# Kernel tuning notes

Measured on AMD Instinct MI355X. Metric: run time of the kernel, lower is better.

The kernel has to match this reference:

```python
import jax, jax.numpy as jnp
import numpy as np

N = 20000        # number of nodes
E_RAND = 140000  # random edges; self-loops appended to match original (neighbors.extend([curr_node]))
D_IN = 512
D_OUT = 512
SLOPE = 0.2


def setup_inputs() -> dict:
    key = jax.random.key(0)
    k1, k2, k3, k4 = jax.random.split(key, 4)
    nodes = jax.random.normal(k1, (N, D_IN), dtype=jnp.float32)
    ei = jax.random.randint(k2, (2, E_RAND), 0, N, dtype=jnp.int64)
    loops = jnp.arange(N, dtype=jnp.int64)
    edge_index = jnp.concatenate([ei, jnp.stack([loops, loops])], axis=1)  # [2, E_RAND+N]
    # learned params: nn.Linear(input_dim, output_dim) and nn.Linear(2*output_dim, 1)
    W = jax.random.normal(k3, (D_IN, D_OUT), dtype=jnp.float32) * (1.0 / np.sqrt(D_IN))
    b_w = jnp.zeros((D_OUT,), dtype=jnp.float32)
    a = jax.random.normal(k4, (2 * D_OUT,), dtype=jnp.float32) * (1.0 / np.sqrt(2 * D_OUT))
    b_a = jnp.zeros((), dtype=jnp.float32)
    return {"nodes": nodes, "edge_index": edge_index, "W": W, "b_w": b_w, "a": a, "b_a": b_a}


def reference(nodes, edge_index, W, b_w, a, b_a):
    # h = W x  (nn.Linear)
    h = nodes @ W + b_w                       # [N, D_OUT]
    src = edge_index[0]                       # neighbor j
    dst = edge_index[1]                       # center   i
    # a([h_i || h_j]) split into per-node partial scores (avoids materializing concat)
    s_dst = h @ a[:D_OUT]                     # [N]
    s_src = h @ a[D_OUT:]                     # [N]
    e = jax.nn.leaky_relu(s_dst[dst] + s_src[src] + b_a, negative_slope=SLOPE)  # [E]
    w = jnp.exp(e)                            # original uses exp without max-shift
    denom = jax.ops.segment_sum(w, dst, num_segments=N)       # [N]
    alpha = w / denom[dst]                    # per-edge softmax weight
    out = jax.ops.segment_sum(alpha[:, None] * h[src], dst, num_segments=N)  # [N, D_OUT]
    return out
```

## Files before the change

### kernel.cpp

```cpp
#include <hip/hip_runtime.h>
#include <stdint.h>

#define D 512
#define SLOPE 0.2f
#define ELLW 64

typedef unsigned short u16;
typedef u16 u16x8 __attribute__((ext_vector_type(8)));
typedef __bf16 bf16x8 __attribute__((ext_vector_type(8)));
typedef float f32x4 __attribute__((ext_vector_type(4)));

__device__ inline float bf2f(u16 b) {
    union { uint32_t u; float f; } v; v.u = ((uint32_t)b) << 16; return v.f;
}
__device__ inline u16 f2bf(float f) {
    union { uint32_t u; float f; } v; v.f = f;
    uint32_t u = v.u;
    if ((u & 0x7F800000u) == 0x7F800000u) return (u16)(u >> 16);
    uint32_t r = u + 0x7FFFu + ((u >> 16) & 1u);
    return (u16)(r >> 16);
}
__device__ inline void load8(const void* X, int isf32, size_t base, float* o) {
    if (isf32) {
        const float4* p = (const float4*)((const float*)X + base);
        float4 a = p[0], b = p[1];
        o[0] = a.x; o[1] = a.y; o[2] = a.z; o[3] = a.w;
        o[4] = b.x; o[5] = b.y; o[6] = b.z; o[7] = b.w;
    } else {
        u16x8 v = *(const u16x8*)((const u16*)X + base);
#pragma unroll
        for (int j = 0; j < 8; j++) o[j] = bf2f(v[j]);
    }
}
__device__ inline float load1(const void* X, int isf32, size_t idx) {
    return isf32 ? ((const float*)X)[idx] : bf2f(((const u16*)X)[idx]);
}
__device__ inline int eload(const void* ei, int is64, size_t idx) {
    return is64 ? (int)((const long long*)ei)[idx] : ((const int*)ei)[idx];
}

__global__ void fill_constf(float* __restrict__ out, float val, int n) {
    int i = blockIdx.x * 256 + threadIdx.x;
    if (i < n) out[i] = val;
}

__global__ void detect2_kernel(const u16* __restrict__ xr, const uint32_t* __restrict__ er,
                               const void* __restrict__ ei, int* __restrict__ flags,
                               int nx, int newords, int E, int Nn) {
    __shared__ int cnt_band, cnt_zero, bad;
    int t = threadIdx.x;
    if (t == 0) { cnt_band = 0; cnt_zero = 0; bad = 0; }
    __syncthreads();
    {
        size_t stride = (size_t)nx / 256;
        size_t idx = ((size_t)t * stride) & ~(size_t)1;
        u16 v = xr[idx];
        int e = (v >> 7) & 0xFF;
        if (e >= 100 && e <= 140) atomicAdd(&cnt_band, 1);
    }
    if (t < 128) {
        size_t stride = (size_t)newords / 128;
        size_t idx = ((size_t)t * stride) | 1;
        if (er[idx] == 0u) atomicAdd(&cnt_zero, 1);
    }
    __syncthreads();
    int i64 = (cnt_zero == 128) ? 1 : 0;
    {
        int base = E - Nn;
        int idx = (t * 613) % Nn;
        if (eload(ei, i64, (size_t)base + idx) != idx) atomicAdd(&bad, 1);
        if (eload(ei, i64, (size_t)E + base + idx) != idx) atomicAdd(&bad, 1);
    }
    __syncthreads();
    if (t == 0) {
        flags[0] = (cnt_band < 200) ? 1 : 0;
        flags[1] = i64;
        flags[2] = (bad == 0) ? 1 : 0;
    }
}

__global__ void prep_kernel(const void* __restrict__ W, const void* __restrict__ bw,
                            const void* __restrict__ a, const int* __restrict__ flags,
                            float* __restrict__ wa_d, float* __restrict__ wa_s,
                            float* __restrict__ cval, int* __restrict__ counts, int Nn) {
    int gid = blockIdx.x * 256 + threadIdx.x;
    if (gid < Nn) counts[gid] = 0;
    int f = flags[0];
    int wave = threadIdx.x >> 6, lane = threadIdx.x & 63;
    int r = blockIdx.x * 4 + wave;
    if (r > D) return;
    float wv[8], ad[8], as[8];
    if (r < D) load8(W, f, (size_t)r * D + lane * 8, wv);
    else       load8(bw, f, (size_t)lane * 8, wv);
    load8(a, f, (size_t)lane * 8, ad);
    load8(a, f, (size_t)D + lane * 8, as);
    float accd = 0.0f, accs = 0.0f;
#pragma unroll
    for (int j = 0; j < 8; j++) {
        accd += wv[j] * ad[j];
        accs += wv[j] * as[j];
    }
#pragma unroll
    for (int m = 1; m < 64; m <<= 1) {
        accd += __shfl_xor(accd, m);
        accs += __shfl_xor(accs, m);
    }
    if (lane == 0) {
        if (r < D) { wa_d[r] = accd; wa_s[r] = accs; }
        else       { cval[0] = accd; cval[1] = accs; }
    }
}


__global__ void score_kernel(const void* __restrict__ X, const int* __restrict__ flags,
                             const float* __restrict__ wa_d, const float* __restrict__ wa_s,
                             const float* __restrict__ cval,
                             float* __restrict__ sd, float* __restrict__ ss, int Nn) {
    int f = flags[0];
    int wave = threadIdx.x >> 6, lane = threadIdx.x & 63;
    int row = blockIdx.x * 4 + wave;
    if (row >= Nn) return;
    float xv[8];
    load8(X, f, (size_t)row * D + lane * 8, xv);
    float accd = 0.0f, accs = 0.0f;
#pragma unroll
    for (int j = 0; j < 8; j++) {
        accd += xv[j] * wa_d[lane * 8 + j];
        accs += xv[j] * wa_s[lane * 8 + j];
    }
#pragma unroll
    for (int m = 1; m < 64; m <<= 1) {
        accd += __shfl_xor(accd, m);
        accs += __shfl_xor(accs, m);
    }
    if (lane == 0) { sd[row] = accd + cval[0]; ss[row] = accs + cval[1]; }
}

__global__ void hist_kernel(const void* __restrict__ ei, const int* __restrict__ flags,
                            int* __restrict__ counts, int E, int Nn) {
    int k = blockIdx.x * 256 + threadIdx.x;
    if (k >= E) return;
    int i64 = flags[1];
    int s = eload(ei, i64, k);
    int d = eload(ei, i64, (size_t)E + k);
    if ((unsigned)s < (unsigned)Nn && (unsigned)d < (unsigned)Nn)
        atomicAdd(&counts[d], 1);
}

__global__ void scan_kernel(const int* __restrict__ counts, int* __restrict__ offsets,
                            int* __restrict__ cursor, int Nn) {
    __shared__ int sm[1024];
    int t = threadIdx.x;
    int per = (Nn + 1023) >> 10;
    int beg = t * per;
    int end = beg + per;
    if (beg > Nn) beg = Nn;
    if (end > Nn) end = Nn;
    int s = 0;
    for (int i = beg; i < end; i++) s += counts[i];
    sm[t] = s;
    __syncthreads();
    for (int off = 1; off < 1024; off <<= 1) {
        int v = (t >= off) ? sm[t - off] : 0;
        __syncthreads();
        sm[t] += v;
        __syncthreads();
    }
    int run = sm[t] - s;
    for (int i = beg; i < end; i++) {
        int c = counts[i];
        offsets[i] = run;
        cursor[i] = run;
        run += c;
    }
    if (beg < Nn && end == Nn) offsets[Nn] = run;
}

__global__ void scatter_kernel(const void* __restrict__ ei, const int* __restrict__ flags,
                               int* __restrict__ cursor, int* __restrict__ esrc,
                               int E, int Nn) {
    int k = blockIdx.x * 256 + threadIdx.x;
    if (k >= E) return;
    int i64 = flags[1];
    int s = eload(ei, i64, k);
    int d = eload(ei, i64, (size_t)E + k);
    if ((unsigned)s >= (unsigned)Nn || (unsigned)d >= (unsigned)Nn) return;
    int pos = atomicAdd(&cursor[d], 1);
    esrc[pos] = s;
}

__global__ void gather_kernel(const void* __restrict__ X, const void* __restrict__ ba_p,
                              const int* __restrict__ flags,
                              const float* __restrict__ sd, const float* __restrict__ ss,
                              const int* __restrict__ offsets, const int* __restrict__ esrc,
                              float* __restrict__ OUT, int Nn) {
    int wave = threadIdx.x >> 6, lane = threadIdx.x & 63;
    int i = blockIdx.x * 4 + wave;
    if (i >= Nn) return;
    int f = flags[0];
    float ba = load1(ba_p, f, 0);
    float sdi = sd[i];
    int beg = offsets[i], end = offsets[i + 1];
    float acc[8] = {0, 0, 0, 0, 0, 0, 0, 0};
    float den = 0.0f;
    for (int e = beg; e < end; e++) {
        int s = esrc[e];
        float ee = sdi + ss[s] + ba;
        ee = (ee > 0.0f) ? ee : SLOPE * ee;
        ee = fminf(fmaxf(ee, -80.0f), 80.0f);
        float w = expf(ee);
        den += w;
        float xv[8];
        load8(X, f, (size_t)s * D + lane * 8, xv);
#pragma unroll
        for (int j = 0; j < 8; j++) acc[j] += w * xv[j];
    }
    float inv = (den > 0.0f) ? 1.0f / den : 0.0f;
    float4 o0, o1;
    o0.x = acc[0] * inv; o0.y = acc[1] * inv; o0.z = acc[2] * inv; o0.w = acc[3] * inv;
    o1.x = acc[4] * inv; o1.y = acc[5] * inv; o1.z = acc[6] * inv; o1.w = acc[7] * inv;
    float* op = OUT + (size_t)i * D + lane * 8;
    *(float4*)op = o0;
    *(float4*)(op + 4) = o1;
}

#define GM 32
#define LDP 40

__global__ __launch_bounds__(256) void gemm2_kernel(
        const u16* __restrict__ WTb, const void* __restrict__ bw,
        const int* __restrict__ flags, float* __restrict__ IO, int M) {
    __shared__ u16 smA[GM * LDP];
    __shared__ u16 smW[D * LDP];
    int f = flags[0];
    int ok = flags[2];
    int t = threadIdx.x;
    int wave = t >> 6, lane = t & 63;
    int lm = lane & 15, q = lane >> 4;
    int tileM = blockIdx.x * GM;

    f32x4 acc[2][8];
#pragma unroll
    for (int mi = 0; mi < 2; mi++)
#pragma unroll
        for (int ni = 0; ni < 8; ni++)
#pragma unroll
            for (int r = 0; r < 4; r++) acc[mi][ni][r] = 0.0f;

    for (int kk = 0; kk < D; kk += 32) {
        {
            int r = t >> 3, c4 = (t & 7) * 4;
            int gr = tileM + r;
            u16 o[4] = {0, 0, 0, 0};
            if (gr < M) {
                float4 v = *(const float4*)(IO + (size_t)gr * D + kk + c4);
                o[0] = f2bf(v.x); o[1] = f2bf(v.y); o[2] = f2bf(v.z); o[3] = f2bf(v.w);
            }
            *(ushort2*)(smA + r * LDP + c4) = make_ushort2(o[0], o[1]);
            *(ushort2*)(smA + r * LDP + c4 + 2) = make_ushort2(o[2], o[3]);
        }
        for (int i = 0; i < 8; i++) {
            int idx = t + i * 256;
            int n = idx >> 2, c8 = (idx & 3) * 8;
            *(u16x8*)(smW + n * LDP + c8) =
                *(const u16x8*)(WTb + (size_t)n * D + kk + c8);
        }
        __syncthreads();

        bf16x8 af[2];
#pragma unroll
        for (int mi = 0; mi < 2; mi++) {
            u16x8 u = *(const u16x8*)(smA + (mi * 16 + lm) * LDP + q * 8);
            union { u16x8 u; bf16x8 b; } cv; cv.u = u;
            af[mi] = cv.b;
        }
#pragma unroll
        for (int ni = 0; ni < 8; ni++) {
            int n = wave * 128 + ni * 16 + lm;
            u16x8 ub = *(const u16x8*)(smW + n * LDP + q * 8);
            union { u16x8 u; bf16x8 b; } cv; cv.u = ub;
            acc[0][ni] = __builtin_amdgcn_mfma_f32_16x16x32_bf16(af[0], cv.b, acc[0][ni], 0, 0, 0);
            acc[1][ni] = __builtin_amdgcn_mfma_f32_16x16x32_bf16(af[1], cv.b, acc[1][ni], 0, 0, 0);
        }
        __syncthreads();
    }

#pragma unroll
    for (int mi = 0; mi < 2; mi++) {
#pragma unroll
        for (int ni = 0; ni < 8; ni++) {
            int col = wave * 128 + ni * 16 + lm;
            float b = load1(bw, f, col);
#pragma unroll
            for (int r = 0; r < 4; r++) {
                int row = tileM + mi * 16 + q * 4 + r;
                if (row < M)
                    IO[(size_t)row * D + col] = ok ? (acc[mi][ni][r] + b) : 512.0f;
            }
        }
    }
}


__global__ void xscore_kernel(const void* __restrict__ X, const int* __restrict__ flags,
                              const float* __restrict__ wa_d, const float* __restrict__ wa_s,
                              const float* __restrict__ cval, u16* __restrict__ Xb,
                              float* __restrict__ sd, float* __restrict__ ss, int Nn) {
    int f = flags[0];
    int wave = threadIdx.x >> 6, lane = threadIdx.x & 63;
    int row = blockIdx.x * 4 + wave;
    if (row >= Nn) return;
    float xv[8];
    load8(X, f, (size_t)row * D + lane * 8, xv);
    u16x8 ov;
#pragma unroll
    for (int j = 0; j < 8; j++) ov[j] = f2bf(xv[j]);
    *(u16x8*)(Xb + (size_t)row * D + lane * 8) = ov;
    float accd = 0.0f, accs = 0.0f;
#pragma unroll
    for (int j = 0; j < 8; j++) {
        accd += xv[j] * wa_d[lane * 8 + j];
        accs += xv[j] * wa_s[lane * 8 + j];
    }
#pragma unroll
    for (int m = 1; m < 64; m <<= 1) {
        accd += __shfl_xor(accd, m);
        accs += __shfl_xor(accs, m);
    }
    if (lane == 0) { sd[row] = accd + cval[0]; ss[row] = accs + cval[1]; }
}

__global__ void scatter3_kernel(const void* __restrict__ ei, int* __restrict__ flags,
                                const float* __restrict__ sd, const float* __restrict__ ss,
                                const void* __restrict__ ba_p, int* __restrict__ counts,
                                int2* __restrict__ epk, int E, int Nn) {
    int k = blockIdx.x * 256 + threadIdx.x;
    if (k >= E) return;
    int i64 = flags[1];
    int s = eload(ei, i64, k);
    int d = eload(ei, i64, (size_t)E + k);
    if ((unsigned)s >= (unsigned)Nn || (unsigned)d >= (unsigned)Nn) return;
    float ba = load1(ba_p, flags[0], 0);
    float ee = sd[d] + ss[s] + ba;
    ee = (ee > 0.0f) ? ee : SLOPE * ee;
    ee = fminf(fmaxf(ee, -80.0f), 80.0f);
    float w = expf(ee);
    int slot = atomicAdd(&counts[d], 1);
    if (slot < ELLW) {
        int2 pk; pk.x = s; pk.y = __float_as_int(w);
        epk[(size_t)d * ELLW + slot] = pk;
    } else {
        atomicAnd(&flags[2], 0);
    }
}

__global__ void gather3_kernel(const u16* __restrict__ Xb, const int2* __restrict__ epk,
                               const int* __restrict__ counts, u16* __restrict__ Hb, int Nn) {
    int wave = threadIdx.x >> 6, lane = threadIdx.x & 63;
    int i = blockIdx.x * 4 + wave;
    if (i >= Nn) return;
    int cnt = counts[i];
    if (cnt > ELLW) cnt = ELLW;
    int2 mypk = make_int2(0, 0);
    if (lane < cnt) mypk = epk[(size_t)i * ELLW + lane];
    float acc[8] = {0, 0, 0, 0, 0, 0, 0, 0};
    float den = 0.0f;
    int e = 0;
    for (; e + 3 < cnt; e += 4) {
        int s0 = __shfl(mypk.x, e);
        int s1 = __shfl(mypk.x, e + 1);
        int s2 = __shfl(mypk.x, e + 2);
        int s3 = __shfl(mypk.x, e + 3);
        float w0 = __int_as_float(__shfl(mypk.y, e));
        float w1 = __int_as_float(__shfl(mypk.y, e + 1));
        float w2 = __int_as_float(__shfl(mypk.y, e + 2));
        float w3 = __int_as_float(__shfl(mypk.y, e + 3));
        u16x8 v0 = *(const u16x8*)(Xb + (size_t)s0 * D + lane * 8);
        u16x8 v1 = *(const u16x8*)(Xb + (size_t)s1 * D + lane * 8);
        u16x8 v2 = *(const u16x8*)(Xb + (size_t)s2 * D + lane * 8);
        u16x8 v3 = *(const u16x8*)(Xb + (size_t)s3 * D + lane * 8);
        den += (w0 + w1) + (w2 + w3);
#pragma unroll
        for (int j = 0; j < 8; j++)
            acc[j] += (w0 * bf2f(v0[j]) + w1 * bf2f(v1[j])) +
                      (w2 * bf2f(v2[j]) + w3 * bf2f(v3[j]));
    }
    for (; e < cnt; e++) {
        int s0 = __shfl(mypk.x, e);
        float w0 = __int_as_float(__shfl(mypk.y, e));
        u16x8 v0 = *(const u16x8*)(Xb + (size_t)s0 * D + lane * 8);
        den += w0;
#pragma unroll
        for (int j = 0; j < 8; j++) acc[j] += w0 * bf2f(v0[j]);
    }
    float inv = (den > 0.0f) ? 1.0f / den : 0.0f;
    u16x8 ov;
#pragma unroll
    for (int j = 0; j < 8; j++) ov[j] = f2bf(acc[j] * inv);
    *(u16x8*)(Hb + (size_t)i * D + lane * 8) = ov;
}

__global__ void wtconv2_kernel(const void* __restrict__ W, const int* __restrict__ flags,
                               u16* __restrict__ WTb) {
    __shared__ __align__(16) u16 sm[64][72];
    int f = flags[0];
    int k0 = blockIdx.x * 64, n0 = blockIdx.y * 64;
    int t = threadIdx.x;
    int kr = t >> 2, c0 = (t & 3) * 16;
    float v[16];
    load8(W, f, (size_t)(k0 + kr) * D + n0 + c0, v);
    load8(W, f, (size_t)(k0 + kr) * D + n0 + c0 + 8, v + 8);
#pragma unroll
    for (int j = 0; j < 16; j++) sm[c0 + j][kr] = f2bf(v[j]);
    __syncthreads();
    int nr = t >> 2, kc0 = (t & 3) * 16;
    u16x8 o0, o1;
#pragma unroll
    for (int j = 0; j < 8; j++) { o0[j] = sm[nr][kc0 + j]; o1[j] = sm[nr][kc0 + 8 + j]; }
    *(u16x8*)(WTb + (size_t)(n0 + nr) * D + k0 + kc0) = o0;
    *(u16x8*)(WTb + (size_t)(n0 + nr) * D + k0 + kc0 + 8) = o1;
}

#define BM3 128
#define BN3 128
#define BK3 32
#define LDP3 40

__global__ __launch_bounds__(256) void gemm3_kernel(
        const u16* __restrict__ Hb, const u16* __restrict__ WTb,
        const void* __restrict__ bw, const int* __restrict__ flags,
        float* __restrict__ OUT, int M) {
    __shared__ __align__(16) u16 smA[BM3 * LDP3];
    __shared__ __align__(16) u16 smB[BN3 * LDP3];
    int f = flags[0];
    int ok = flags[2];
    int t = threadIdx.x;
    int wave = t >> 6, lane = t & 63;
    int lm = lane & 15, q = lane >> 4;
    int wm = wave >> 1, wn = wave & 1;
    int tileM = blockIdx.x * BM3;
    int tileN = blockIdx.y * BN3;

    f32x4 acc[4][4];
#pragma unroll
    for (int mi = 0; mi < 4; mi++)
#pragma unroll
        for (int ni = 0; ni < 4; ni++)
#pragma unroll
            for (int r = 0; r < 4; r++) acc[mi][ni][r] = 0.0f;

    int sr0 = t >> 2, sc0 = (t & 3) * 8;
    int sr1 = sr0 + 64;
    int gr0 = tileM + sr0; if (gr0 >= M) gr0 = M - 1;
    int gr1 = tileM + sr1; if (gr1 >= M) gr1 = M - 1;
    const u16* gA0 = Hb + (size_t)gr0 * D + sc0;
    const u16* gA1 = Hb + (size_t)gr1 * D + sc0;
    const u16* gB0 = WTb + (size_t)(tileN + sr0) * D + sc0;
    const u16* gB1 = WTb + (size_t)(tileN + sr1) * D + sc0;
    u16* lA0 = smA + sr0 * LDP3 + sc0;
    u16* lA1 = smA + sr1 * LDP3 + sc0;
    u16* lB0 = smB + sr0 * LDP3 + sc0;
    u16* lB1 = smB + sr1 * LDP3 + sc0;

    for (int kk = 0; kk < D; kk += BK3) {
        *(u16x8*)lA0 = *(const u16x8*)(gA0 + kk);
        *(u16x8*)lA1 = *(const u16x8*)(gA1 + kk);
        *(u16x8*)lB0 = *(const u16x8*)(gB0 + kk);
        *(u16x8*)lB1 = *(const u16x8*)(gB1 + kk);
        __syncthreads();

        bf16x8 af[4], bfr[4];
#pragma unroll
        for (int mi = 0; mi < 4; mi++) {
            int r = wm * 64 + mi * 16 + lm;
            union { u16x8 u; bf16x8 b; } cv;
            cv.u = *(const u16x8*)(smA + r * LDP3 + q * 8);
            af[mi] = cv.b;
        }
#pragma unroll
        for (int ni = 0; ni < 4; ni++) {
            int n = wn * 64 + ni * 16 + lm;
            union { u16x8 u; bf16x8 b; } cv;
            cv.u = *(const u16x8*)(smB + n * LDP3 + q * 8);
            bfr[ni] = cv.b;
        }
#pragma unroll
        for (int mi = 0; mi < 4; mi++)
#pragma unroll
            for (int ni = 0; ni < 4; ni++)
                acc[mi][ni] = __builtin_amdgcn_mfma_f32_16x16x32_bf16(
                    af[mi], bfr[ni], acc[mi][ni], 0, 0, 0);
        __syncthreads();
    }

#pragma unroll
    for (int ni = 0; ni < 4; ni++) {
        int col = tileN + wn * 64 + ni * 16 + lm;
        float b = load1(bw, f, col);
#pragma unroll
        for (int mi = 0; mi < 4; mi++) {
            int row0 = tileM + wm * 64 + mi * 16 + q * 4;
#pragma unroll
            for (int r = 0; r < 4; r++) {
                int row = row0 + r;
                if (row < M)
                    OUT[(size_t)row * D + col] = ok ? (acc[mi][ni][r] + b) : 512.0f;
            }
        }
    }
}

extern "C" void kernel_launch(void* const* d_in, const int* in_sizes, int n_in,
                              void* d_out, int out_size, void* d_ws, size_t ws_size,
                              hipStream_t stream) {
    float* out = (float*)d_out;
    int nOut = out_size;
    auto fill = [&](float v) {
        fill_constf<<<(nOut + 255) / 256, 256, 0, stream>>>(out, v, nOut);
    };
    if (n_in != 6) { fill(1024.0f); return; }
    const int exp_sizes[6] = {20000 * 512, 2 * 160000, 512 * 512, 512, 1024, 1};
    for (int i = 0; i < 6; i++)
        if (in_sizes[i] != exp_sizes[i]) { fill(2048.0f); return; }
    for (int i = 0; i < 6; i++)
        if (((uintptr_t)d_in[i]) & 15) { fill(8192.0f); return; }
    if ((((uintptr_t)d_out) & 15) || (((uintptr_t)d_ws) & 15)) { fill(8192.0f); return; }

    const void* nodes = d_in[0];
    const void* ei    = d_in[1];
    const void* W     = d_in[2];
    const void* bw    = d_in[3];
    const void* a     = d_in[4];
    const void* ba    = d_in[5];

    int Nn = in_sizes[0] / D;
    int E  = in_sizes[1] / 2;

    char* p = (char*)d_ws;
    auto alloc = [&](size_t bytes) {
        char* r = p;
        p += (bytes + 255) & ~(size_t)255;
        return r;
    };
    float* sd      = (float*)alloc((size_t)Nn * 4);
    float* ss      = (float*)alloc((size_t)Nn * 4);
    int*   counts  = (int*)alloc((size_t)Nn * 4);
    int*   offsets = (int*)alloc((size_t)(Nn + 1) * 4);
    int*   cursor  = (int*)alloc((size_t)Nn * 4);
    int*   esrc    = (int*)alloc((size_t)E * 4);
    u16*   WTb     = (u16*)alloc((size_t)D * D * 2);
    float* wa_d    = (float*)alloc((size_t)D * 4);
    float* wa_s    = (float*)alloc((size_t)D * 4);
    float* cval    = (float*)alloc(256);
    int*   flags   = (int*)alloc(256);
    if ((size_t)(p - (char*)d_ws) > ws_size) { fill(4096.0f); return; }

    size_t xbB  = (size_t)Nn * D * 2;
    size_t epkB = (size_t)Nn * ELLW * 8;
    size_t bigNeed = ((xbB + 255) & ~(size_t)255) * 2 + ((epkB + 255) & ~(size_t)255);
    bool fast = ((size_t)(p - (char*)d_ws) + bigNeed) <= ws_size;
    u16* Xb = nullptr; u16* Hb = nullptr; int2* epk = nullptr;
    if (fast) {
        Xb  = (u16*)alloc(xbB);
        Hb  = (u16*)alloc(xbB);
        epk = (int2*)alloc(epkB);
    }

    detect2_kernel<<<1, 256, 0, stream>>>((const u16*)nodes, (const uint32_t*)ei, ei,
                                          flags, in_sizes[0], in_sizes[1], E, Nn);
    prep_kernel<<<(D + 1 + 3) / 4, 256, 0, stream>>>(W, bw, a, flags, wa_d, wa_s, cval,
                                                     counts, Nn);

    if (fast) {
        xscore_kernel<<<(Nn + 3) / 4, 256, 0, stream>>>(nodes, flags, wa_d, wa_s, cval,
                                                        Xb, sd, ss, Nn);
        scatter3_kernel<<<(E + 255) / 256, 256, 0, stream>>>(ei, flags, sd, ss, ba,
                                                             counts, epk, E, Nn);
        wtconv2_kernel<<<dim3(D / 64, D / 64), 256, 0, stream>>>(W, flags, WTb);
        gather3_kernel<<<(Nn + 3) / 4, 256, 0, stream>>>(Xb, epk, counts, Hb, Nn);
        gemm3_kernel<<<dim3((Nn + BM3 - 1) / BM3, D / BN3), 256, 0, stream>>>(
            Hb, WTb, bw, flags, out, Nn);
    } else {
        score_kernel<<<(Nn + 3) / 4, 256, 0, stream>>>(nodes, flags, wa_d, wa_s, cval,
                                                       sd, ss, Nn);
        hist_kernel<<<(E + 255) / 256, 256, 0, stream>>>(ei, flags, counts, E, Nn);
        scan_kernel<<<1, 1024, 0, stream>>>(counts, offsets, cursor, Nn);
        scatter_kernel<<<(E + 255) / 256, 256, 0, stream>>>(ei, flags, cursor, esrc, E, Nn);
        wtconv2_kernel<<<dim3(D / 64, D / 64), 256, 0, stream>>>(W, flags, WTb);
        gather_kernel<<<(Nn + 3) / 4, 256, 0, stream>>>(nodes, ba, flags, sd, ss,
                                                        offsets, esrc, out, Nn);
        gemm2_kernel<<<(Nn + GM - 1) / GM, 256, 0, stream>>>(WTb, bw, flags, out, Nn);
    }
}
```

Before: 173.3 us.

## Fuse W transpose into prep, unroll gather by 8, use direct global-to-LDS loads in GEMM

Folds the W transpose/bf16 conversion into the prep kernel so one launch is removed. Adds an 8-way unrolled edge loop in the gather so more row loads are in flight per wave. Changes the GEMM's tile staging to global_load_lds with an XOR-swizzled unpadded LDS layout, skipping the register round trip. The swizzle must match the load pattern exactly, and the unroll raises register pressure.

Result: faster. 167.2 us (-3.5%).

```diff
diff --git a/kernel.cpp b/kernel.cpp
--- a/kernel.cpp
+++ b/kernel.cpp
@@ -37,6 +37,13 @@
 }
 __device__ inline int eload(const void* ei, int is64, size_t idx) {
     return is64 ? (int)((const long long*)ei)[idx] : ((const int*)ei)[idx];
+}
+
+__device__ inline void gload_lds16(const u16* g, u16* l) {
+    __builtin_amdgcn_global_load_lds(
+        (const __attribute__((address_space(1))) uint32_t*)g,
+        (__attribute__((address_space(3))) uint32_t*)l,
+        16, 0, 0);
 }
 
 __global__ void fill_constf(float* __restrict__ out, float val, int n) {
@@ -79,35 +86,56 @@
     }
 }
 
-__global__ void prep_kernel(const void* __restrict__ W, const void* __restrict__ bw,
-                            const void* __restrict__ a, const int* __restrict__ flags,
-                            float* __restrict__ wa_d, float* __restrict__ wa_s,
-                            float* __restrict__ cval, int* __restrict__ counts, int Nn) {
-    int gid = blockIdx.x * 256 + threadIdx.x;
+__global__ void prep2_kernel(const void* __restrict__ W, const void* __restrict__ bw,
+                             const void* __restrict__ a, const int* __restrict__ flags,
+                             float* __restrict__ wa_d, float* __restrict__ wa_s,
+                             float* __restrict__ cval, int* __restrict__ counts,
+                             u16* __restrict__ WTb, int Nn) {
+    __shared__ __align__(16) u16 sm[64][72];
+    int bid = blockIdx.x;
+    int t = threadIdx.x;
+    int gid = bid * 256 + t;
     if (gid < Nn) counts[gid] = 0;
     int f = flags[0];
-    int wave = threadIdx.x >> 6, lane = threadIdx.x & 63;
-    int r = blockIdx.x * 4 + wave;
-    if (r > D) return;
-    float wv[8], ad[8], as[8];
-    if (r < D) load8(W, f, (size_t)r * D + lane * 8, wv);
-    else       load8(bw, f, (size_t)lane * 8, wv);
-    load8(a, f, (size_t)lane * 8, ad);
-    load8(a, f, (size_t)D + lane * 8, as);
-    float accd = 0.0f, accs = 0.0f;
-#pragma unroll
-    for (int j = 0; j < 8; j++) {
-        accd += wv[j] * ad[j];
-        accs += wv[j] * as[j];
-    }
-#pragma unroll
-    for (int m = 1; m < 64; m <<= 1) {
-        accd += __shfl_xor(accd, m);
-        accs += __shfl_xor(accs, m);
-    }
-    if (lane == 0) {
-        if (r < D) { wa_d[r] = accd; wa_s[r] = accs; }
-        else       { cval[0] = accd; cval[1] = accs; }
+    if (bid < 64) {
+        int k0 = (bid & 7) * 64, n0 = (bid >> 3) * 64;
+        int kr = t >> 2, c0 = (t & 3) * 16;
+        float v[16];
+        load8(W, f, (size_t)(k0 + kr) * D + n0 + c0, v);
+        load8(W, f, (size_t)(k0 + kr) * D + n0 + c0 + 8, v + 8);
+#pragma unroll
+        for (int j = 0; j < 16; j++) sm[c0 + j][kr] = f2bf(v[j]);
+        __syncthreads();
+        int nr = t >> 2, kc0 = (t & 3) * 16;
+        u16x8 o0, o1;
+#pragma unroll
+        for (int j = 0; j < 8; j++) { o0[j] = sm[nr][kc0 + j]; o1[j] = sm[nr][kc0 + 8 + j]; }
+        *(u16x8*)(WTb + (size_t)(n0 + nr) * D + k0 + kc0) = o0;
+        *(u16x8*)(WTb + (size_t)(n0 + nr) * D + k0 + kc0 + 8) = o1;
+    } else {
+        int wave = t >> 6, lane = t & 63;
+        int r = (bid - 64) * 4 + wave;
+        if (r > D) return;
+        float wv[8], ad[8], as[8];
+        if (r < D) load8(W, f, (size_t)r * D + lane * 8, wv);
+        else       load8(bw, f, (size_t)lane * 8, wv);
+        load8(a, f, (size_t)lane * 8, ad);
+        load8(a, f, (size_t)D + lane * 8, as);
+        float accd = 0.0f, accs = 0.0f;
+#pragma unroll
+        for (int j = 0; j < 8; j++) {
+            accd += wv[j] * ad[j];
+            accs += wv[j] * as[j];
+        }
+#pragma unroll
+        for (int m = 1; m < 64; m <<= 1) {
+            accd += __shfl_xor(accd, m);
+            accs += __shfl_xor(accs, m);
+        }
+        if (lane == 0) {
+            if (r < D) { wa_d[r] = accd; wa_s[r] = accs; }
+            else       { cval[0] = accd; cval[1] = accs; }
+        }
     }
 }
 
@@ -366,6 +394,28 @@
     float acc[8] = {0, 0, 0, 0, 0, 0, 0, 0};
     float den = 0.0f;
     int e = 0;
+    for (; e + 7 < cnt; e += 8) {
+        int s_[8]; float w_[8];
+#pragma unroll
+        for (int u = 0; u < 8; u++) {
+            s_[u] = __shfl(mypk.x, e + u);
+            w_[u] = __int_as_float(__shfl(mypk.y, e + u));
+        }
+        u16x8 v_[8];
+#pragma unroll
+        for (int u = 0; u < 8; u++)
+            v_[u] = *(const u16x8*)(Xb + (size_t)s_[u] * D + lane * 8);
+#pragma unroll
+        for (int u = 0; u < 8; u++) den += w_[u];
+#pragma unroll
+        for (int j = 0; j < 8; j++) {
+            float t0 = w_[0] * bf2f(v_[0][j]) + w_[1] * bf2f(v_[1][j]);
+            float t1 = w_[2] * bf2f(v_[2][j]) + w_[3] * bf2f(v_[3][j]);
+            float t2 = w_[4] * bf2f(v_[4][j]) + w_[5] * bf2f(v_[5][j]);
+            float t3 = w_[6] * bf2f(v_[6][j]) + w_[7] * bf2f(v_[7][j]);
+            acc[j] += (t0 + t1) + (t2 + t3);
+        }
+    }
     for (; e + 3 < cnt; e += 4) {
         int s0 = __shfl(mypk.x, e);
         int s1 = __shfl(mypk.x, e + 1);
@@ -400,38 +450,15 @@
     *(u16x8*)(Hb + (size_t)i * D + lane * 8) = ov;
 }
 
-__global__ void wtconv2_kernel(const void* __restrict__ W, const int* __restrict__ flags,
-                               u16* __restrict__ WTb) {
-    __shared__ __align__(16) u16 sm[64][72];
-    int f = flags[0];
-    int k0 = blockIdx.x * 64, n0 = blockIdx.y * 64;
-    int t = threadIdx.x;
-    int kr = t >> 2, c0 = (t & 3) * 16;
-    float v[16];
-    load8(W, f, (size_t)(k0 + kr) * D + n0 + c0, v);
-    load8(W, f, (size_t)(k0 + kr) * D + n0 + c0 + 8, v + 8);
-#pragma unroll
-    for (int j = 0; j < 16; j++) sm[c0 + j][kr] = f2bf(v[j]);
-    __syncthreads();
-    int nr = t >> 2, kc0 = (t & 3) * 16;
-    u16x8 o0, o1;
-#pragma unroll
-    for (int j = 0; j < 8; j++) { o0[j] = sm[nr][kc0 + j]; o1[j] = sm[nr][kc0 + 8 + j]; }
-    *(u16x8*)(WTb + (size_t)(n0 + nr) * D + k0 + kc0) = o0;
-    *(u16x8*)(WTb + (size_t)(n0 + nr) * D + k0 + kc0 + 8) = o1;
-}
-
 #define BM3 128
 #define BN3 128
-#define BK3 32
-#define LDP3 40
 
 __global__ __launch_bounds__(256) void gemm3_kernel(
         const u16* __restrict__ Hb, const u16* __restrict__ WTb,
         const void* __restrict__ bw, const int* __restrict__ flags,
         float* __restrict__ OUT, int M) {
-    __shared__ __align__(16) u16 smA[BM3 * LDP3];
-    __shared__ __align__(16) u16 smB[BN3 * LDP3];
+    __shared__ __align__(16) u16 smA[BM3 * 32];
+    __shared__ __align__(16) u16 smB[BN3 * 32];
     int f = flags[0];
     int ok = flags[2];
     int t = threadIdx.x;
@@ -449,24 +476,28 @@
 #pragma unroll
             for (int r = 0; r < 4; r++) acc[mi][ni][r] = 0.0f;
 
-    int sr0 = t >> 2, sc0 = (t & 3) * 8;
-    int sr1 = sr0 + 64;
-    int gr0 = tileM + sr0; if (gr0 >= M) gr0 = M - 1;
-    int gr1 = tileM + sr1; if (gr1 >= M) gr1 = M - 1;
-    const u16* gA0 = Hb + (size_t)gr0 * D + sc0;
-    const u16* gA1 = Hb + (size_t)gr1 * D + sc0;
-    const u16* gB0 = WTb + (size_t)(tileN + sr0) * D + sc0;
-    const u16* gB1 = WTb + (size_t)(tileN + sr1) * D + sc0;
-    u16* lA0 = smA + sr0 * LDP3 + sc0;
-    u16* lA1 = smA + sr1 * LDP3 + sc0;
-    u16* lB0 = smB + sr0 * LDP3 + sc0;
-    u16* lB1 = smB + sr1 * LDP3 + sc0;
-
-    for (int kk = 0; kk < D; kk += BK3) {
-        *(u16x8*)lA0 = *(const u16x8*)(gA0 + kk);
-        *(u16x8*)lA1 = *(const u16x8*)(gA1 + kk);
-        *(u16x8*)lB0 = *(const u16x8*)(gB0 + kk);
-        *(u16x8*)lB1 = *(const u16x8*)(gB1 + kk);
+    int k8 = (lane & 3) ^ ((lane >> 3) & 3);
+    int rsub = lane >> 2;
+    int c0 = wave * 2, c1 = wave * 2 + 1;
+    int rA0 = c0 * 16 + rsub, rA1 = c1 * 16 + rsub;
+    int gA0 = tileM + rA0; if (gA0 >= M) gA0 = M - 1;
+    int gA1 = tileM + rA1; if (gA1 >= M) gA1 = M - 1;
+    const u16* srcA0 = Hb + (size_t)gA0 * D + k8 * 8;
+    const u16* srcA1 = Hb + (size_t)gA1 * D + k8 * 8;
+    const u16* srcB0 = WTb + (size_t)(tileN + rA0) * D + k8 * 8;
+    const u16* srcB1 = WTb + (size_t)(tileN + rA1) * D + k8 * 8;
+    u16* dA0 = smA + c0 * 512;
+    u16* dA1 = smA + c1 * 512;
+    u16* dB0 = smB + c0 * 512;
+    u16* dB1 = smB + c1 * 512;
+
+    int jq = q ^ ((lm >> 1) & 3);
+
+    for (int kk = 0; kk < D; kk += 32) {
+        gload_lds16(srcA0 + kk, dA0);
+        gload_lds16(srcA1 + kk, dA1);
+        gload_lds16(srcB0 + kk, dB0);
+        gload_lds16(srcB1 + kk, dB1);
         __syncthreads();
 
         bf16x8 af[4], bfr[4];
@@ -474,14 +505,14 @@
         for (int mi = 0; mi < 4; mi++) {
             int r = wm * 64 + mi * 16 + lm;
             union { u16x8 u; bf16x8 b; } cv;
-            cv.u = *(const u16x8*)(smA + r * LDP3 + q * 8);
+            cv.u = *(const u16x8*)(smA + r * 32 + jq * 8);
             af[mi] = cv.b;
         }
 #pragma unroll
         for (int ni = 0; ni < 4; ni++) {
             int n = wn * 64 + ni * 16 + lm;
             union { u16x8 u; bf16x8 b; } cv;
-            cv.u = *(const u16x8*)(smB + n * LDP3 + q * 8);
+            cv.u = *(const u16x8*)(smB + n * 32 + jq * 8);
             bfr[ni] = cv.b;
         }
 #pragma unroll
@@ -568,15 +599,14 @@
 
     detect2_kernel<<<1, 256, 0, stream>>>((const u16*)nodes, (const uint32_t*)ei, ei,
                                           flags, in_sizes[0], in_sizes[1], E, Nn);
-    prep_kernel<<<(D + 1 + 3) / 4, 256, 0, stream>>>(W, bw, a, flags, wa_d, wa_s, cval,
-                                                     counts, Nn);
+    prep2_kernel<<<64 + 129, 256, 0, stream>>>(W, bw, a, flags, wa_d, wa_s, cval,
+                                               counts, WTb, Nn);
 
     if (fast) {
         xscore_kernel<<<(Nn + 3) / 4, 256, 0, stream>>>(nodes, flags, wa_d, wa_s, cval,
                                                         Xb, sd, ss, Nn);
         scatter3_kernel<<<(E + 255) / 256, 256, 0, stream>>>(ei, flags, sd, ss, ba,
                                                              counts, epk, E, Nn);
-        wtconv2_kernel<<<dim3(D / 64, D / 64), 256, 0, stream>>>(W, flags, WTb);
         gather3_kernel<<<(Nn + 3) / 4, 256, 0, stream>>>(Xb, epk, counts, Hb, Nn);
         gemm3_kernel<<<dim3((Nn + BM3 - 1) / BM3, D / BN3), 256, 0, stream>>>(
             Hb, WTb, bw, flags, out, Nn);
@@ -586,7 +616,6 @@
         hist_kernel<<<(E + 255) / 256, 256, 0, stream>>>(ei, flags, counts, E, Nn);
         scan_kernel<<<1, 1024, 0, stream>>>(counts, offsets, cursor, Nn);
         scatter_kernel<<<(E + 255) / 256, 256, 0, stream>>>(ei, flags, cursor, esrc, E, Nn);
-        wtconv2_kernel<<<dim3(D / 64, D / 64), 256, 0, stream>>>(W, flags, WTb);
         gather_kernel<<<(Nn + 3) / 4, 256, 0, stream>>>(nodes, ba, flags, sd, ss,
                                                         offsets, esrc, out, Nn);
         gemm2_kernel<<<(Nn + GM - 1) / GM, 256, 0, stream>>>(WTb, bw, flags, out, Nn);
```
